# Kernel optimization log

Measured on AMD Instinct MI355X. Metric: run time of the kernel, lower is better.

The kernel has to match this reference:

```python
import jax, jax.numpy as jnp
import numpy as np

H = 8  # num_heads in both MHA blocks


def _mha_self(x, W_in, b_in, W_out, b_out, mask=None):
    """Faithful nn.MultiheadAttention self-attention (batch_first).
    x: [B,S,E]; W_in: [3E,E]; b_in: [3E]; W_out: [E,E]; b_out: [E].
    mask: optional [S,S] bool, True = attend."""
    B, S, E = x.shape
    dh = E // H
    qkv = x @ W_in.T + b_in                      # [B,S,3E]
    q, k, v = jnp.split(qkv, 3, axis=-1)
    # [B,H,S,dh]
    q = q.reshape(B, S, H, dh).transpose(0, 2, 1, 3)
    k = k.reshape(B, S, H, dh).transpose(0, 2, 1, 3)
    v = v.reshape(B, S, H, dh).transpose(0, 2, 1, 3)
    scores = jnp.einsum('bhqd,bhkd->bhqk', q, k) / jnp.sqrt(jnp.asarray(dh, x.dtype))
    if mask is not None:
        scores = jnp.where(mask[None, None], scores, jnp.finfo(scores.dtype).min)
    probs = jax.nn.softmax(scores, axis=-1)
    out = jnp.einsum('bhqk,bhkd->bhqd', probs, v)  # [B,H,S,dh]
    out = out.transpose(0, 2, 1, 3).reshape(B, S, E)
    return out @ W_out.T + b_out


def setup_inputs() -> dict:
    key = jax.random.key(0)
    ks = jax.random.split(key, 7)
    B, S, E = 8, 1024, 512
    sc = 0.02
    return {
        'x': jax.random.normal(ks[0], (B, S, E), jnp.float32),
        'Wl_in': jax.random.normal(ks[1], (3 * E, E), jnp.float32) * sc,
        'bl_in': jnp.zeros((3 * E,), jnp.float32),
        'Wl_out': jax.random.normal(ks[2], (E, E), jnp.float32) * sc,
        'bl_out': jnp.zeros((E,), jnp.float32),
        'Wg_in': jax.random.normal(ks[3], (3 * E, E), jnp.float32) * sc,
        'bg_in': jnp.zeros((3 * E,), jnp.float32),
        'Wg_out': jax.random.normal(ks[4], (E, E), jnp.float32) * sc,
        'bg_out': jnp.zeros((E,), jnp.float32),
        'Wf': jax.random.normal(ks[5], (E, 2 * E), jnp.float32) * sc,
        'bf': jnp.zeros((E,), jnp.float32),
    }


def reference(x, Wl_in, bl_in, Wl_out, bl_out, Wg_in, bg_in, Wg_out, bg_out, Wf, bf):
    LOCAL = 3  # local_size
    B, S, E = x.shape
    # Per-token sliding window [i-LOCAL, i+LOCAL] == banded attention mask
    idx = jnp.arange(S)
    band = jnp.abs(idx[:, None] - idx[None, :]) <= LOCAL  # [S,S] bool
    local_out = _mha_self(x, Wl_in, bl_in, Wl_out, bl_out, mask=band)
    global_out = _mha_self(x, Wg_in, bg_in, Wg_out, bg_out)
    fused = jnp.concatenate([local_out, global_out], axis=-1)  # [B,S,2E]
    return jax.nn.relu(fused @ Wf.T + bf)
```

## Files before the change

### kernel.cpp

```cpp
#include <hip/hip_runtime.h>

typedef unsigned short u16;
typedef unsigned int   u32;
typedef __bf16 v8bf __attribute__((ext_vector_type(8)));
typedef float  v4f  __attribute__((ext_vector_type(4)));
typedef u16    us4  __attribute__((ext_vector_type(4)));
typedef u32    ui4  __attribute__((ext_vector_type(4)));
typedef u32    ui2  __attribute__((ext_vector_type(2)));

__device__ __forceinline__ u16 f2bf(float f) {
  u32 u = __builtin_bit_cast(u32, f);
  u += 0x7fffu + ((u >> 16) & 1u);
  return (u16)(u >> 16);
}
__device__ __forceinline__ float bf2f(u16 s) {
  u32 u = ((u32)s) << 16;
  return __builtin_bit_cast(float, u);
}

__device__ __forceinline__ void load_lds16(const u16* g, u16* l) {
  __builtin_amdgcn_global_load_lds(
      (const __attribute__((address_space(1))) u32*)g,
      (__attribute__((address_space(3))) u32*)l, 16, 0, 0);
}

__global__ void __launch_bounds__(256) cvt_all(
    const float* __restrict__ x,   const float* __restrict__ wli,
    const float* __restrict__ wlo, const float* __restrict__ wgi,
    const float* __restrict__ wgo, const float* __restrict__ wf,
    u16* __restrict__ out, u16* __restrict__ wloT, u16* __restrict__ wgoT)
{
  const int v = blockIdx.x * 256 + threadIdx.x;
  const float* src; int obase; int mode = 0; u16* T = nullptr;
  if      (v < 1048576) { src = x;   obase = 0;       }
  else if (v < 1245184) { src = wli; obase = 1048576; }
  else if (v < 1310720) { src = wlo; obase = 1245184; mode = 1; T = wloT; }
  else if (v < 1507328) { src = wgi; obase = 1310720; }
  else if (v < 1572864) { src = wgo; obase = 1507328; mode = 1; T = wgoT; }
  else                  { src = wf;  obase = 1572864; }
  const int rel = v - obase;
  const float4 f = reinterpret_cast<const float4*>(src)[rel];
  us4 o;
  o.x = f2bf(f.x); o.y = f2bf(f.y); o.z = f2bf(f.z); o.w = f2bf(f.w);
  if (mode) {
    const int eb = rel * 4, c = eb >> 9, k = eb & 511;
#pragma unroll
    for (int i = 0; i < 4; ++i) T[(k + i) * 512 + c] = o[i];
  } else {
    int o4;
    if      (v < 1245184) o4 = v;
    else if (v < 1507328) o4 = v - 65536;
    else                  o4 = v - 131072;
    reinterpret_cast<us4*>(out)[o4] = o;
  }
}

template<int RELU, int OUTF32, int TV, int BIASF>
__device__ __forceinline__ void gemm_body(
    u16* __restrict__ As, u16* __restrict__ Bs,
    const u16* __restrict__ A, const int lda,
    const u16* __restrict__ B, const int ldb,
    const float* __restrict__ bias, void* __restrict__ C,
    u16* __restrict__ vt, const int bm, const int bn,
    const int K, const int ldc, const int colofs)
{
  const int tid  = threadIdx.x;
  const int lane = tid & 63;
  const int w    = tid >> 6;
  const int lid  = lane & 15;
  const int quad = lane >> 4;
  const int wr = w >> 1, wc = w & 1;

  v4f acc[4][4];
#pragma unroll
  for (int i = 0; i < 4; ++i)
#pragma unroll
    for (int j = 0; j < 4; ++j)
      acc[i][j] = (v4f){0.f, 0.f, 0.f, 0.f};

  const int dr = lane >> 3;
  const int cs = ((lane ^ dr) & 7) * 8;

  for (int k0 = 0; k0 < K; k0 += 64) {
#pragma unroll
    for (int p = 0; p < 4; ++p) {
      const int g   = w + p * 4;
      const int row = g * 8 + dr;
      load_lds16(A + (size_t)(bm + row) * lda + k0 + cs, As + g * 512);
      load_lds16(B + (size_t)(bn + row) * ldb + k0 + cs, Bs + g * 512);
    }
    __syncthreads();
#pragma unroll
    for (int kk = 0; kk < 2; ++kk) {
      v8bf af[4], bfr[4];
#pragma unroll
      for (int mi = 0; mi < 4; ++mi)
        af[mi] = *reinterpret_cast<const v8bf*>(
            &As[(wr * 64 + mi * 16 + lid) * 64 + (((kk * 4 + quad) ^ (lid & 7)) * 8)]);
#pragma unroll
      for (int ni = 0; ni < 4; ++ni)
        bfr[ni] = *reinterpret_cast<const v8bf*>(
            &Bs[(wc * 64 + ni * 16 + lid) * 64 + (((kk * 4 + quad) ^ (lid & 7)) * 8)]);
#pragma unroll
      for (int mi = 0; mi < 4; ++mi)
#pragma unroll
        for (int ni = 0; ni < 4; ++ni)
          acc[mi][ni] = __builtin_amdgcn_mfma_f32_16x16x32_bf16(
              af[mi], bfr[ni], acc[mi][ni], 0, 0, 0);
    }
    __syncthreads();
  }

  float bv[4];
#pragma unroll
  for (int ni = 0; ni < 4; ++ni)
    bv[ni] = BIASF ? bias[bn + wc * 64 + ni * 16 + lid] : 0.f;

  if (TV && bn >= 1024) {
#pragma unroll
    for (int mi = 0; mi < 4; ++mi) {
      const int m0 = bm + wr * 64 + mi * 16 + quad * 4;
#pragma unroll
      for (int ni = 0; ni < 4; ++ni) {
        const int n = bn + wc * 64 + ni * 16 + lid - 1024;
        us4 pk;
#pragma unroll
        for (int r = 0; r < 4; ++r) pk[r] = f2bf(acc[mi][ni][r] + bv[ni]);
        const size_t idx =
            ((size_t)((m0 >> 10) * 8 + (n >> 6)) * 64 + (n & 63)) * 1024 + (m0 & 1023);
        *reinterpret_cast<us4*>(&vt[idx]) = pk;
      }
    }
  } else {
#pragma unroll
    for (int mi = 0; mi < 4; ++mi) {
#pragma unroll
      for (int ni = 0; ni < 4; ++ni) {
        const int n = bn + wc * 64 + ni * 16 + lid;
#pragma unroll
        for (int r = 0; r < 4; ++r) {
          const int m = bm + wr * 64 + mi * 16 + quad * 4 + r;
          float v = acc[mi][ni][r] + bv[ni];
          if (RELU) v = fmaxf(v, 0.f);
          if (OUTF32)
            reinterpret_cast<float*>(C)[(size_t)m * ldc + colofs + n] = v;
          else
            reinterpret_cast<u16*>(C)[(size_t)m * ldc + colofs + n] = f2bf(v);
        }
      }
    }
  }
}

__global__ void __launch_bounds__(256) qkv_dual(
    const u16* __restrict__ xb,
    const u16* __restrict__ wli, const float* __restrict__ bli, u16* __restrict__ qkv_l,
    const u16* __restrict__ wgi, const float* __restrict__ bgi, u16* __restrict__ qkv_g,
    u16* __restrict__ vt)
{
  __shared__ __align__(16) u16 As[128 * 64];
  __shared__ __align__(16) u16 Bs[128 * 64];
  if (blockIdx.x < 12)
    gemm_body<0,0,0,1>(As, Bs, xb, 512, wli, 512, bli, qkv_l, nullptr,
                       blockIdx.y * 128, blockIdx.x * 128, 512, 1536, 0);
  else
    gemm_body<0,0,1,1>(As, Bs, xb, 512, wgi, 512, bgi, qkv_g, vt,
                       blockIdx.y * 128, (blockIdx.x - 12) * 128, 512, 1536, 0);
}

__global__ void __launch_bounds__(256, 3) mega(
    const u16* __restrict__ qkv, const u16* __restrict__ vt, u16* __restrict__ outp,
    const u16* __restrict__ wfb, const u16* __restrict__ wloT, const u16* __restrict__ wgoT,
    u16* __restrict__ Wc, const float* __restrict__ blo, const float* __restrict__ bgo,
    const float* __restrict__ bff, float* __restrict__ bias_c,
    const u16* __restrict__ qkvl, u16* __restrict__ attn_l)
{
  __shared__ __align__(16) u16 smem[24576];
  const int bx   = blockIdx.x;
  const int tid  = threadIdx.x;
  const int lane = tid & 63;
  const int w    = tid >> 6;

  if (bx >= 552) {
    const int lbx = bx - 552;
    const int qt = lbx & 15, bh = lbx >> 4;
    const int b = bh >> 3, h = bh & 7;
    const int i0 = qt * 64;
    const size_t base = (size_t)b * 1024 * 1536;
    u16* Kl = smem;
    u16* Vl = smem + 5040;

    for (int i2 = tid; i2 < 1120; i2 += 256) {
      const int isV = i2 >= 560;
      const int i3  = isV ? i2 - 560 : i2;
      const int row = i3 >> 3, ch = i3 & 7;
      const int jc = min(max(i0 - 3 + row, 0), 1023);
      const ui4 d = *reinterpret_cast<const ui4*>(
          qkvl + base + (size_t)jc * 1536 + (isV ? 1024 : 512) + h * 64 + ch * 8);
      *reinterpret_cast<ui4*>(&(isV ? Vl : Kl)[row * 72 + ch * 8]) = d;
    }
    __syncthreads();

    const int q   = lane >> 2;
    const int oct = lane & 3;
    const int i   = i0 + w * 16 + q;
    const u16* qrow = qkvl + base + (size_t)i * 1536 + h * 64 + oct * 16;
    float qf[16];
    {
      const v8bf q0 = *reinterpret_cast<const v8bf*>(qrow);
      const v8bf q1 = *reinterpret_cast<const v8bf*>(qrow + 8);
#pragma unroll
      for (int e = 0; e < 8; ++e) { qf[e] = (float)q0[e]; qf[8 + e] = (float)q1[e]; }
    }
    float denom = 0.f, accv[16];
#pragma unroll
    for (int e = 0; e < 16; ++e) accv[e] = 0.f;

#pragma unroll
    for (int tt = 0; tt < 7; ++tt) {
      const int j = i - 3 + tt;
      const bool ok = (j >= 0) && (j <= 1023);
      const int ridx = w * 16 + q + tt;
      const v8bf k0 = *reinterpret_cast<const v8bf*>(&Kl[ridx * 72 + oct * 16]);
      const v8bf k1 = *reinterpret_cast<const v8bf*>(&Kl[ridx * 72 + oct * 16 + 8]);
      float pr = 0.f;
#pragma unroll
      for (int e = 0; e < 8; ++e)
        pr += qf[e] * (float)k0[e] + qf[8 + e] * (float)k1[e];
      pr += __shfl_xor(pr, 1);
      pr += __shfl_xor(pr, 2);
      const float p = ok ? __expf(pr * 0.125f) : 0.f;
      denom += p;
      const v8bf v0 = *reinterpret_cast<const v8bf*>(&Vl[ridx * 72 + oct * 16]);
      const v8bf v1 = *reinterpret_cast<const v8bf*>(&Vl[ridx * 72 + oct * 16 + 8]);
#pragma unroll
      for (int e = 0; e < 8; ++e) {
        accv[e]     += p * (float)v0[e];
        accv[8 + e] += p * (float)v1[e];
      }
    }
    const float inv = 1.f / denom;
    u16* dst = attn_l + (size_t)(b * 1024 + i) * 1536 + h * 64 + oct * 16;
#pragma unroll
    for (int c4 = 0; c4 < 4; ++c4) {
      us4 pk;
#pragma unroll
      for (int e = 0; e < 4; ++e) pk[e] = f2bf(accv[c4 * 4 + e] * inv);
      *reinterpret_cast<us4*>(dst + c4 * 4) = pk;
    }
    return;
  }
  if (bx >= 544) {
    const int e = (bx - 544) * 64 + w * 16;
    for (int t = 0; t < 16; ++t) {
      float sum = 0.f;
#pragma unroll
      for (int j = 0; j < 16; ++j) {
        const int c2 = j * 64 + lane;
        const float b = (c2 < 512) ? blo[c2] : bgo[c2 - 512];
        sum += bf2f(wfb[(size_t)(e + t) * 1024 + c2]) * b;
      }
#pragma unroll
      for (int msk = 32; msk >= 1; msk >>= 1) sum += __shfl_xor(sum, msk);
      if (lane == 0) bias_c[e + t] = bff[e + t] + sum;
    }
    return;
  }
  if (bx >= 512) {
    const int idx = bx - 512;
    const int half = idx >> 4, rem = idx & 15;
    gemm_body<0,0,0,0>(smem, smem + 8192, wfb + half * 512, 1024,
                       (half ? wgoT : wloT), 512, nullptr, Wc, nullptr,
                       (rem >> 2) * 128, (rem & 3) * 128, 512, 1024, half * 512);
    return;
  }

  const int lid  = lane & 15;
  const int quad = lane >> 4;
  const int qt = (bx >> 3) & 7;
  const int bh = ((bx & 7) << 3) | (bx >> 6);
  const int b = bh >> 3, h = bh & 7;
  const size_t base = (size_t)b * 1024 * 1536;

  v8bf aq[2][2];
#pragma unroll
  for (int qs = 0; qs < 2; ++qs) {
    const size_t qoff =
        base + (size_t)(qt * 128 + w * 32 + qs * 16 + lid) * 1536 + h * 64 + quad * 8;
    aq[qs][0] = *reinterpret_cast<const v8bf*>(qkv + qoff);
    aq[qs][1] = *reinterpret_cast<const v8bf*>(qkv + qoff + 32);
#pragma unroll
    for (int k = 0; k < 2; ++k)
#pragma unroll
      for (int i = 0; i < 8; ++i)
        aq[qs][k][i] = (__bf16)((float)aq[qs][k][i] * 0.125f);
  }
  v8bf ones;
#pragma unroll
  for (int i = 0; i < 8; ++i) ones[i] = (__bf16)1.0f;

  v4f o[2][4], lacc[2];
#pragma unroll
  for (int qs = 0; qs < 2; ++qs) {
    lacc[qs] = (v4f){0.f, 0.f, 0.f, 0.f};
#pragma unroll
    for (int nd = 0; nd < 4; ++nd) o[qs][nd] = (v4f){0.f, 0.f, 0.f, 0.f};
  }

  u16* Ps = smem + 16384;
  const int dr = lane >> 3;
  const int dc = lane & 7;
#define STAGE(KT, BI)                                                          \
  {                                                                            \
    _Pragma("unroll") for (int p = 0; p < 2; ++p) {                            \
      const int r = (w + p * 4) * 8 + dr;                                      \
      const int cs = (dc ^ (r & 7)) * 8;                                       \
      load_lds16(qkv + base + (size_t)((KT) * 64 + r) * 1536 + 512 + h * 64 + cs, \
                 smem + (BI) * 4096 + (w + p * 4) * 512);                      \
      load_lds16(vt + ((size_t)bh * 64 + r) * 1024 + (KT) * 64 + cs,           \
                 smem + 8192 + (BI) * 4096 + (w + p * 4) * 512);               \
    }                                                                          \
  }
  STAGE(0, 0);

  for (int kt = 0; kt < 16; ++kt) {
    __syncthreads();
    if (kt < 15) STAGE(kt + 1, (kt + 1) & 1);
    const u16* Ks = smem + (kt & 1) * 4096;
    const u16* Vs = smem + 8192 + (kt & 1) * 4096;

    v8bf bk[2][4];
#pragma unroll
    for (int kk = 0; kk < 2; ++kk)
#pragma unroll
      for (int nk = 0; nk < 4; ++nk)
        bk[kk][nk] = *reinterpret_cast<const v8bf*>(
            &Ks[(nk * 16 + lid) * 64 + (((kk * 4 + quad) ^ (lid & 7)) * 8)]);

#pragma unroll
    for (int qs = 0; qs < 2; ++qs) {
      v4f s[4];
#pragma unroll
      for (int nk = 0; nk < 4; ++nk) s[nk] = (v4f){0.f, 0.f, 0.f, 0.f};
#pragma unroll
      for (int kk = 0; kk < 2; ++kk)
#pragma unroll
        for (int nk = 0; nk < 4; ++nk)
          s[nk] = __builtin_amdgcn_mfma_f32_16x16x32_bf16(
              bk[kk][nk], aq[qs][kk], s[nk], 0, 0, 0);
#pragma unroll
      for (int nk = 0; nk < 4; ++nk) {
        const u32 b0 = __builtin_bit_cast(u32, __expf(s[nk][0]));
        const u32 b1 = __builtin_bit_cast(u32, __expf(s[nk][1]));
        const u32 b2 = __builtin_bit_cast(u32, __expf(s[nk][2]));
        const u32 b3 = __builtin_bit_cast(u32, __expf(s[nk][3]));
        ui2 pk;
        pk.x = (b1 & 0xffff0000u) | (b0 >> 16);
        pk.y = (b3 & 0xffff0000u) | (b2 >> 16);
        const int c8 = (nk * 2 + (quad >> 1)) ^ (lid & 7);
        *reinterpret_cast<ui2*>(
            &Ps[w * 2048 + qs * 1024 + lid * 64 + c8 * 8 + (quad & 1) * 4]) = pk;
      }
    }

#pragma unroll
    for (int kk = 0; kk < 2; ++kk) {
      v8bf av[4];
#pragma unroll
      for (int nd = 0; nd < 4; ++nd)
        av[nd] = *reinterpret_cast<const v8bf*>(
            &Vs[(nd * 16 + lid) * 64 + (((kk * 4 + quad) ^ (lid & 7)) * 8)]);
#pragma unroll
      for (int qs = 0; qs < 2; ++qs) {
        const v8bf ap = *reinterpret_cast<const v8bf*>(
            &Ps[w * 2048 + qs * 1024 + lid * 64 + (((kk * 4 + quad) ^ (lid & 7)) * 8)]);
        lacc[qs] = __builtin_amdgcn_mfma_f32_16x16x32_bf16(ones, ap, lacc[qs], 0, 0, 0);
#pragma unroll
        for (int nd = 0; nd < 4; ++nd)
          o[qs][nd] = __builtin_amdgcn_mfma_f32_16x16x32_bf16(
              av[nd], ap, o[qs][nd], 0, 0, 0);
      }
    }
  }
#undef STAGE

#pragma unroll
  for (int qs = 0; qs < 2; ++qs) {
    const float inv = 1.f / lacc[qs][0];
    const int tok = b * 1024 + qt * 128 + w * 32 + qs * 16 + lid;
#pragma unroll
    for (int nd = 0; nd < 4; ++nd) {
      us4 pk;
#pragma unroll
      for (int r = 0; r < 4; ++r) pk[r] = f2bf(o[qs][nd][r] * inv);
      *reinterpret_cast<us4*>(
          &outp[(size_t)tok * 512 + h * 64 + nd * 16 + quad * 4]) = pk;
    }
  }
}

__global__ void __launch_bounds__(256) gemm_final(
    const u16* __restrict__ Al, const u16* __restrict__ Ag,
    const u16* __restrict__ Bw, const float* __restrict__ biasc,
    float* __restrict__ out)
{
  __shared__ __align__(16) u16 As[64 * 64];
  __shared__ __align__(16) u16 Bs[128 * 64];
  const int tid  = threadIdx.x;
  const int lane = tid & 63;
  const int w    = tid >> 6;
  const int lid  = lane & 15;
  const int quad = lane >> 4;
  const int bm = blockIdx.y * 64;
  const int bn = blockIdx.x * 128;

  v4f acc[4][2];
#pragma unroll
  for (int i = 0; i < 4; ++i)
#pragma unroll
    for (int j = 0; j < 2; ++j)
      acc[i][j] = (v4f){0.f, 0.f, 0.f, 0.f};

  const int dr = lane >> 3;
  const int cs = ((lane ^ dr) & 7) * 8;

  for (int k0 = 0; k0 < 1024; k0 += 64) {
    const int half = k0 >> 9;
    const u16* Asrc = half ? Ag : Al;
    const int  lda  = half ? 512 : 1536;
    const int  kcol = k0 & 511;
#pragma unroll
    for (int p = 0; p < 2; ++p) {
      const int g   = w + p * 4;
      const int row = g * 8 + dr;
      load_lds16(Asrc + (size_t)(bm + row) * lda + kcol + cs, As + g * 512);
    }
#pragma unroll
    for (int p = 0; p < 4; ++p) {
      const int g   = w + p * 4;
      const int row = g * 8 + dr;
      load_lds16(Bw + (size_t)(bn + row) * 1024 + k0 + cs, Bs + g * 512);
    }
    __syncthreads();
#pragma unroll
    for (int kk = 0; kk < 2; ++kk) {
      v8bf af[4], bfr[2];
#pragma unroll
      for (int mi = 0; mi < 4; ++mi)
        af[mi] = *reinterpret_cast<const v8bf*>(
            &As[(mi * 16 + lid) * 64 + (((kk * 4 + quad) ^ (lid & 7)) * 8)]);
#pragma unroll
      for (int ni = 0; ni < 2; ++ni)
        bfr[ni] = *reinterpret_cast<const v8bf*>(
            &Bs[(w * 32 + ni * 16 + lid) * 64 + (((kk * 4 + quad) ^ (lid & 7)) * 8)]);
#pragma unroll
      for (int mi = 0; mi < 4; ++mi)
#pragma unroll
        for (int ni = 0; ni < 2; ++ni)
          acc[mi][ni] = __builtin_amdgcn_mfma_f32_16x16x32_bf16(
              af[mi], bfr[ni], acc[mi][ni], 0, 0, 0);
    }
    __syncthreads();
  }

#pragma unroll
  for (int mi = 0; mi < 4; ++mi) {
#pragma unroll
    for (int ni = 0; ni < 2; ++ni) {
      const int n = bn + w * 32 + ni * 16 + lid;
      const float bv = biasc[n];
#pragma unroll
      for (int r = 0; r < 4; ++r) {
        const int m = bm + mi * 16 + quad * 4 + r;
        out[(size_t)m * 512 + n] = fmaxf(acc[mi][ni][r] + bv, 0.f);
      }
    }
  }
}

extern "C" void kernel_launch(void* const* d_in, const int* in_sizes, int n_in,
                              void* d_out, int out_size, void* d_ws, size_t ws_size,
                              hipStream_t stream) {
  (void)in_sizes; (void)n_in; (void)out_size; (void)ws_size;
  const float* x   = (const float*)d_in[0];
  const float* Wli = (const float*)d_in[1];
  const float* bli = (const float*)d_in[2];
  const float* Wlo = (const float*)d_in[3];
  const float* blo = (const float*)d_in[4];
  const float* Wgi = (const float*)d_in[5];
  const float* bgi = (const float*)d_in[6];
  const float* Wgo = (const float*)d_in[7];
  const float* bgo = (const float*)d_in[8];
  const float* Wf  = (const float*)d_in[9];
  const float* bff = (const float*)d_in[10];
  float* out = (float*)d_out;

  u16* W      = (u16*)d_ws;
  u16* xb     = W + 0;
  u16* wli    = W + 4194304;
  u16* wgi    = W + 4980736;
  u16* wfb    = W + 5767168;
  u16* qkv_l  = W + 6291456;
  u16* qkv_g  = W + 18874368;
  u16* vt     = W + 31457280;
  u16* Wc     = W + 35651584;
  float* bias_c = (float*)(W + 36175872);
  u16* wloT   = W + 36176896;
  u16* wgoT   = W + 36439040;
  u16* attn_g = W + 0;
  u16* attn_l = qkv_g + 1024;

  cvt_all<<<6656, 256, 0, stream>>>(x, Wli, Wlo, Wgi, Wgo, Wf, W, wloT, wgoT);
  qkv_dual<<<dim3(24, 64), 256, 0, stream>>>(xb, wli, bli, qkv_l, wgi, bgi, qkv_g, vt);
  mega<<<1576, 256, 0, stream>>>(qkv_g, vt, attn_g, wfb, wloT, wgoT, Wc,
                                 blo, bgo, bff, bias_c, qkv_l, attn_l);
  gemm_final<<<dim3(4, 128), 256, 0, stream>>>(attn_l, attn_g, Wc, bias_c, out);
}
```

Measured before the change: 177.5 us.

## Load GEMM fragments directly from global memory, bypassing LDS staging

The QKV projection GEMM and the final fused GEMM now load MFMA operand fragments straight from global memory into registers, with no LDS tiles and no barriers. The weight-combine GEMM inside the mega kernel keeps LDS staging through a new specialised copy of the old body. The goal is to remove LDS round-trips and __syncthreads stalls and let memory latency overlap across waves. The cost is redundant global/L2 reads (each wave reloads data that blocks used to share), loads that are less coalesced, and higher register pressure.

```diff
diff --git a/kernel.cpp b/kernel.cpp
--- a/kernel.cpp
+++ b/kernel.cpp
@@ -55,12 +55,11 @@
   }
 }
 
-template<int RELU, int OUTF32, int TV, int BIASF>
-__device__ __forceinline__ void gemm_body(
-    u16* __restrict__ As, u16* __restrict__ Bs,
+template<int TV, int BIASF>
+__device__ __forceinline__ void gemm_direct(
     const u16* __restrict__ A, const int lda,
     const u16* __restrict__ B, const int ldb,
-    const float* __restrict__ bias, void* __restrict__ C,
+    const float* __restrict__ bias, u16* __restrict__ C,
     u16* __restrict__ vt, const int bm, const int bn,
     const int K, const int ldc, const int colofs)
 {
@@ -78,37 +77,31 @@
     for (int j = 0; j < 4; ++j)
       acc[i][j] = (v4f){0.f, 0.f, 0.f, 0.f};
 
-  const int dr = lane >> 3;
-  const int cs = ((lane ^ dr) & 7) * 8;
+  const u16* Ap = A + (size_t)(bm + wr * 64 + lid) * lda + quad * 8;
+  const u16* Bp = B + (size_t)(bn + wc * 64 + lid) * ldb + quad * 8;
 
   for (int k0 = 0; k0 < K; k0 += 64) {
-#pragma unroll
-    for (int p = 0; p < 4; ++p) {
-      const int g   = w + p * 4;
-      const int row = g * 8 + dr;
-      load_lds16(A + (size_t)(bm + row) * lda + k0 + cs, As + g * 512);
-      load_lds16(B + (size_t)(bn + row) * ldb + k0 + cs, Bs + g * 512);
-    }
-    __syncthreads();
-#pragma unroll
-    for (int kk = 0; kk < 2; ++kk) {
-      v8bf af[4], bfr[4];
+    v8bf af[2][4], bfr[2][4];
+#pragma unroll
+    for (int kk = 0; kk < 2; ++kk)
 #pragma unroll
       for (int mi = 0; mi < 4; ++mi)
-        af[mi] = *reinterpret_cast<const v8bf*>(
-            &As[(wr * 64 + mi * 16 + lid) * 64 + (((kk * 4 + quad) ^ (lid & 7)) * 8)]);
+        af[kk][mi] = *reinterpret_cast<const v8bf*>(
+            Ap + (size_t)mi * 16 * lda + k0 + kk * 32);
+#pragma unroll
+    for (int kk = 0; kk < 2; ++kk)
 #pragma unroll
       for (int ni = 0; ni < 4; ++ni)
-        bfr[ni] = *reinterpret_cast<const v8bf*>(
-            &Bs[(wc * 64 + ni * 16 + lid) * 64 + (((kk * 4 + quad) ^ (lid & 7)) * 8)]);
+        bfr[kk][ni] = *reinterpret_cast<const v8bf*>(
+            Bp + (size_t)ni * 16 * ldb + k0 + kk * 32);
+#pragma unroll
+    for (int kk = 0; kk < 2; ++kk)
 #pragma unroll
       for (int mi = 0; mi < 4; ++mi)
 #pragma unroll
         for (int ni = 0; ni < 4; ++ni)
           acc[mi][ni] = __builtin_amdgcn_mfma_f32_16x16x32_bf16(
-              af[mi], bfr[ni], acc[mi][ni], 0, 0, 0);
-    }
-    __syncthreads();
+              af[kk][mi], bfr[kk][ni], acc[mi][ni], 0, 0, 0);
   }
 
   float bv[4];
@@ -140,12 +133,7 @@
 #pragma unroll
         for (int r = 0; r < 4; ++r) {
           const int m = bm + wr * 64 + mi * 16 + quad * 4 + r;
-          float v = acc[mi][ni][r] + bv[ni];
-          if (RELU) v = fmaxf(v, 0.f);
-          if (OUTF32)
-            reinterpret_cast<float*>(C)[(size_t)m * ldc + colofs + n] = v;
-          else
-            reinterpret_cast<u16*>(C)[(size_t)m * ldc + colofs + n] = f2bf(v);
+          C[(size_t)m * ldc + colofs + n] = f2bf(acc[mi][ni][r] + bv[ni]);
         }
       }
     }
@@ -158,14 +146,80 @@
     const u16* __restrict__ wgi, const float* __restrict__ bgi, u16* __restrict__ qkv_g,
     u16* __restrict__ vt)
 {
-  __shared__ __align__(16) u16 As[128 * 64];
-  __shared__ __align__(16) u16 Bs[128 * 64];
   if (blockIdx.x < 12)
-    gemm_body<0,0,0,1>(As, Bs, xb, 512, wli, 512, bli, qkv_l, nullptr,
-                       blockIdx.y * 128, blockIdx.x * 128, 512, 1536, 0);
+    gemm_direct<0,1>(xb, 512, wli, 512, bli, qkv_l, nullptr,
+                     blockIdx.y * 128, blockIdx.x * 128, 512, 1536, 0);
   else
-    gemm_body<0,0,1,1>(As, Bs, xb, 512, wgi, 512, bgi, qkv_g, vt,
-                       blockIdx.y * 128, (blockIdx.x - 12) * 128, 512, 1536, 0);
+    gemm_direct<1,1>(xb, 512, wgi, 512, bgi, qkv_g, vt,
+                     blockIdx.y * 128, (blockIdx.x - 12) * 128, 512, 1536, 0);
+}
+
+__device__ __forceinline__ void gemm_body_wc(
+    u16* __restrict__ As, u16* __restrict__ Bs,
+    const u16* __restrict__ A, const int lda,
+    const u16* __restrict__ B, const int ldb,
+    u16* __restrict__ C, const int bm, const int bn,
+    const int K, const int ldc, const int colofs)
+{
+  const int tid  = threadIdx.x;
+  const int lane = tid & 63;
+  const int w    = tid >> 6;
+  const int lid  = lane & 15;
+  const int quad = lane >> 4;
+  const int wr = w >> 1, wc = w & 1;
+
+  v4f acc[4][4];
+#pragma unroll
+  for (int i = 0; i < 4; ++i)
+#pragma unroll
+    for (int j = 0; j < 4; ++j)
+      acc[i][j] = (v4f){0.f, 0.f, 0.f, 0.f};
+
+  const int dr = lane >> 3;
+  const int cs = ((lane ^ dr) & 7) * 8;
+
+  for (int k0 = 0; k0 < K; k0 += 64) {
+#pragma unroll
+    for (int p = 0; p < 4; ++p) {
+      const int g   = w + p * 4;
+      const int row = g * 8 + dr;
+      load_lds16(A + (size_t)(bm + row) * lda + k0 + cs, As + g * 512);
+      load_lds16(B + (size_t)(bn + row) * ldb + k0 + cs, Bs + g * 512);
+    }
+    __syncthreads();
+#pragma unroll
+    for (int kk = 0; kk < 2; ++kk) {
+      v8bf af[4], bfr[4];
+#pragma unroll
+      for (int mi = 0; mi < 4; ++mi)
+        af[mi] = *reinterpret_cast<const v8bf*>(
+            &As[(wr * 64 + mi * 16 + lid) * 64 + (((kk * 4 + quad) ^ (lid & 7)) * 8)]);
+#pragma unroll
+      for (int ni = 0; ni < 4; ++ni)
+        bfr[ni] = *reinterpret_cast<const v8bf*>(
+            &Bs[(wc * 64 + ni * 16 + lid) * 64 + (((kk * 4 + quad) ^ (lid & 7)) * 8)]);
+#pragma unroll
+      for (int mi = 0; mi < 4; ++mi)
+#pragma unroll
+        for (int ni = 0; ni < 4; ++ni)
+          acc[mi][ni] = __builtin_amdgcn_mfma_f32_16x16x32_bf16(
+              af[mi], bfr[ni], acc[mi][ni], 0, 0, 0);
+    }
+    __syncthreads();
+  }
+
+#pragma unroll
+  for (int mi = 0; mi < 4; ++mi) {
+#pragma unroll
+    for (int ni = 0; ni < 4; ++ni) {
+      const int n = bn + wc * 64 + ni * 16 + lid;
+#pragma unroll
+      for (int r = 0; r < 4; ++r) {
+        const int m = bm + wr * 64 + mi * 16 + quad * 4 + r;
+        C[(size_t)m * ldc + colofs + n] = f2bf(acc[mi][ni][r]);
+      }
+    }
+  }
 }
 
 __global__ void __launch_bounds__(256, 3) mega(
@@ -269,9 +323,9 @@
   if (bx >= 512) {
     const int idx = bx - 512;
     const int half = idx >> 4, rem = idx & 15;
-    gemm_body<0,0,0,0>(smem, smem + 8192, wfb + half * 512, 1024,
-                       (half ? wgoT : wloT), 512, nullptr, Wc, nullptr,
-                       (rem >> 2) * 128, (rem & 3) * 128, 512, 1024, half * 512);
+    gemm_body_wc(smem, smem + 8192, wfb + half * 512, 1024,
+                 (half ? wgoT : wloT), 512, Wc,
+                 (rem >> 2) * 128, (rem & 3) * 128, 512, 1024, half * 512);
     return;
   }
 
@@ -404,8 +458,6 @@
     const u16* __restrict__ Bw, const float* __restrict__ biasc,
     float* __restrict__ out)
 {
-  __shared__ __align__(16) u16 As[64 * 64];
-  __shared__ __align__(16) u16 Bs[128 * 64];
   const int tid  = threadIdx.x;
   const int lane = tid & 63;
   const int w    = tid >> 6;
@@ -421,46 +473,36 @@
     for (int j = 0; j < 2; ++j)
       acc[i][j] = (v4f){0.f, 0.f, 0.f, 0.f};
 
-  const int dr = lane >> 3;
-  const int cs = ((lane ^ dr) & 7) * 8;
+  const u16* Bp = Bw + (size_t)(bn + w * 32 + lid) * 1024 + quad * 8;
 
   for (int k0 = 0; k0 < 1024; k0 += 64) {
     const int half = k0 >> 9;
     const u16* Asrc = half ? Ag : Al;
     const int  lda  = half ? 512 : 1536;
     const int  kcol = k0 & 511;
-#pragma unroll
-    for (int p = 0; p < 2; ++p) {
-      const int g   = w + p * 4;
-      const int row = g * 8 + dr;
-      load_lds16(Asrc + (size_t)(bm + row) * lda + kcol + cs, As + g * 512);
-    }
-#pragma unroll
-    for (int p = 0; p < 4; ++p) {
-      const int g   = w + p * 4;
-      const int row = g * 8 + dr;
-      load_lds16(Bw + (size_t)(bn + row) * 1024 + k0 + cs, Bs + g * 512);
-    }
-    __syncthreads();
-#pragma unroll
-    for (int kk = 0; kk < 2; ++kk) {
-      v8bf af[4], bfr[2];
+    const u16* Ap = Asrc + (size_t)(bm + lid) * lda + kcol + quad * 8;
+
+    v8bf af[2][4], bfr[2][2];
+#pragma unroll
+    for (int kk = 0; kk < 2; ++kk)
 #pragma unroll
       for (int mi = 0; mi < 4; ++mi)
-        af[mi] = *reinterpret_cast<const v8bf*>(
-            &As[(mi * 16 + lid) * 64 + (((kk * 4 + quad) ^ (lid & 7)) * 8)]);
+        af[kk][mi] = *reinterpret_cast<const v8bf*>(
+            Ap + (size_t)mi * 16 * lda + kk * 32);
+#pragma unroll
+    for (int kk = 0; kk < 2; ++kk)
 #pragma unroll
       for (int ni = 0; ni < 2; ++ni)
-        bfr[ni] = *reinterpret_cast<const v8bf*>(
-            &Bs[(w * 32 + ni * 16 + lid) * 64 + (((kk * 4 + quad) ^ (lid & 7)) * 8)]);
+        bfr[kk][ni] = *reinterpret_cast<const v8bf*>(
+            Bp + (size_t)ni * 16 * 1024 + k0 + kk * 32);
+#pragma unroll
+    for (int kk = 0; kk < 2; ++kk)
 #pragma unroll
       for (int mi = 0; mi < 4; ++mi)
 #pragma unroll
         for (int ni = 0; ni < 2; ++ni)
           acc[mi][ni] = __builtin_amdgcn_mfma_f32_16x16x32_bf16(
-              af[mi], bfr[ni], acc[mi][ni], 0, 0, 0);
-    }
-    __syncthreads();
+              af[kk][mi], bfr[kk][ni], acc[mi][ni], 0, 0, 0);
   }
 
 #pragma unroll
```

Measured after the change: 263.8 us. 48.6% more time.
